# Kernel optimization log

Hardware: AMD Instinct MI355X
Metric: run time of the kernel (lower is better)

## Reference

```python
import jax, jax.numpy as jnp
import numpy as np

N = 100_000            # nodes
E = 1_600_000          # edges per metapath
IN = 256               # input features
HEADS, DIM = 8, 16     # heads * dim = hidden_channels
HIDDEN = HEADS * DIM   # 128
OUT = 4                # classes
NEG_SLOPE = 0.2


def setup_inputs() -> dict:
    key = jax.random.key(0)
    ks = jax.random.split(key, 16)
    s = 1.0 / np.sqrt(HIDDEN)
    return {
        "x": jax.random.normal(ks[0], (N, IN), jnp.float32),
        "edge_index0": jax.random.randint(ks[1], (2, E), 0, N, jnp.int64),
        "edge_index1": jax.random.randint(ks[2], (2, E), 0, N, jnp.int64),
        "proj_w": jax.random.normal(ks[3], (IN, HIDDEN), jnp.float32) / np.sqrt(IN),
        "proj_b": jnp.zeros((HIDDEN,), jnp.float32),
        "att_src0": jax.random.normal(ks[4], (HEADS, DIM), jnp.float32) * s,
        "att_dst0": jax.random.normal(ks[5], (HEADS, DIM), jnp.float32) * s,
        "att_src1": jax.random.normal(ks[6], (HEADS, DIM), jnp.float32) * s,
        "att_dst1": jax.random.normal(ks[7], (HEADS, DIM), jnp.float32) * s,
        "k_lin_w": jax.random.normal(ks[8], (HIDDEN, HIDDEN), jnp.float32) * s,
        "k_lin_b": jnp.zeros((HIDDEN,), jnp.float32),
        "q": jax.random.normal(ks[9], (HIDDEN,), jnp.float32) * s,
        "lin_w": jax.random.normal(ks[10], (HIDDEN, OUT), jnp.float32) * s,
        "lin_b": jnp.zeros((OUT,), jnp.float32),
    }


def _metapath_conv(xp, a_src, a_dst, src, dst):
    # xp: [N,H,D]; a_src, a_dst: [H,D]; src/dst: [E]
    alpha_src = (xp * a_src).sum(-1)                     # [N,H]
    alpha_dst = (xp * a_dst).sum(-1)                     # [N,H]
    e = jax.nn.leaky_relu(alpha_src[src] + alpha_dst[dst], NEG_SLOPE)  # [E,H]
    emax = jax.ops.segment_max(e, dst, num_segments=N)  # [N,H] (stable softmax)
    e = jnp.exp(e - emax[dst])
    denom = jax.ops.segment_sum(e, dst, num_segments=N)
    alpha = e / (denom[dst] + 1e-16)                     # edge softmax per dst
    msg = xp[src] * alpha[..., None]                     # [E,H,D]
    out = jax.ops.segment_sum(msg, dst, num_segments=N)  # [N,H,D]
    return jax.nn.relu(out.reshape(N, HIDDEN))


def reference(x, edge_index0, edge_index1, proj_w, proj_b,
              att_src0, att_dst0, att_src1, att_dst1,
              k_lin_w, k_lin_b, q, lin_w, lin_b):
    # shared node-type projection
    xp = (x @ proj_w + proj_b).reshape(N, HEADS, DIM)
    # per-metapath GAT-style convolutions (dropout=0.6 is eval no-op)
    outs = jnp.stack([
        _metapath_conv(xp, att_src0, att_dst0, edge_index0[0], edge_index0[1]),
        _metapath_conv(xp, att_src1, att_dst1, edge_index1[0], edge_index1[1]),
    ])                                                    # [M,N,HIDDEN]
    # semantic attention over metapaths
    k = jnp.tanh(outs @ k_lin_w + k_lin_b).mean(axis=1)  # [M,HIDDEN]
    attn = jax.nn.softmax((k * q).sum(-1))               # [M]
    fused = (attn[:, None, None] * outs).sum(0)          # [N,HIDDEN]
    return fused @ lin_w + lin_b                          # [N,OUT]
```

## Files before the change

kernel.cpp:

```cpp
#include <hip/hip_runtime.h>
#include <hip/hip_bf16.h>

#define NN 100000
#define EE 1600000
#define HID 128
#define NEG 0.2f
#define CAP 64
#define BSH 9
#define NB 196
#define CAPB 9216
#define EBLK 16384

typedef __attribute__((ext_vector_type(8))) short short8;
typedef __attribute__((ext_vector_type(4))) float f32x4;

__global__ __launch_bounds__(256) void k_proj(const float* __restrict__ x,
    const float* __restrict__ w, const float* __restrict__ bias,
    __hip_bfloat162* __restrict__ xph) {
  __shared__ float xs[64][32];
  __shared__ float ws[32][128];
  const int tid = threadIdx.x;
  const int row0 = blockIdx.x * 64;
  const int cb = (tid & 31) * 4;
  const int rb = (tid >> 5) * 8;
  float acc[8][4] = {};
  for (int k0 = 0; k0 < 256; k0 += 32) {
    {
      int f = tid * 8;
      int r = f >> 5, c = f & 31;
      int rg = row0 + r;
      float4 v0 = make_float4(0.f, 0.f, 0.f, 0.f), v1 = v0;
      if (rg < NN) {
        const float4* src = (const float4*)&x[(size_t)rg * 256 + k0 + c];
        v0 = src[0];
        v1 = src[1];
      }
      *(float4*)&xs[r][c] = v0;
      *(float4*)&xs[r][c + 4] = v1;
    }
    {
      int f = tid * 16;
      int r = f >> 7, c = f & 127;
      const float4* src = (const float4*)&w[(size_t)(k0 + r) * 128 + c];
      float4 a0 = src[0], a1 = src[1], a2 = src[2], a3 = src[3];
      *(float4*)&ws[r][c] = a0;
      *(float4*)&ws[r][c + 4] = a1;
      *(float4*)&ws[r][c + 8] = a2;
      *(float4*)&ws[r][c + 12] = a3;
    }
    __syncthreads();
#pragma unroll
    for (int kk = 0; kk < 32; kk++) {
      float4 wv = *(const float4*)&ws[kk][cb];
#pragma unroll
      for (int r = 0; r < 8; r++) {
        float a = xs[rb + r][kk];
        acc[r][0] = fmaf(a, wv.x, acc[r][0]);
        acc[r][1] = fmaf(a, wv.y, acc[r][1]);
        acc[r][2] = fmaf(a, wv.z, acc[r][2]);
        acc[r][3] = fmaf(a, wv.w, acc[r][3]);
      }
    }
    __syncthreads();
  }
  float4 bv = *(const float4*)&bias[cb];
#pragma unroll
  for (int r = 0; r < 8; r++) {
    int rg = row0 + rb + r;
    if (rg < NN) {
      float4 o;
      o.x = acc[r][0] + bv.x;
      o.y = acc[r][1] + bv.y;
      o.z = acc[r][2] + bv.z;
      o.w = acc[r][3] + bv.w;
      __hip_bfloat162 b01 = __float22bfloat162_rn(make_float2(o.x, o.y));
      __hip_bfloat162 b23 = __float22bfloat162_rn(make_float2(o.z, o.w));
      *(uint2*)&xph[(size_t)rg * 64 + (cb >> 1)] =
          make_uint2(*(unsigned*)&b01, *(unsigned*)&b23);
    }
  }
}

__global__ __launch_bounds__(256) void k_alpha(const __hip_bfloat162* __restrict__ xph,
    const float* __restrict__ a0s, const float* __restrict__ a0d,
    const float* __restrict__ a1s, const float* __restrict__ a1d,
    float* __restrict__ as0, float* __restrict__ ad0,
    float* __restrict__ as1, float* __restrict__ ad1) {
  const int lane = threadIdx.x & 63;
  const int node = blockIdx.x * 4 + (threadIdx.x >> 6);
  if (node >= NN) return;
  float2 v = __bfloat1622float2(xph[(size_t)node * 64 + lane]);
  int i0 = 2 * lane;
  float p0 = v.x * a0s[i0] + v.y * a0s[i0 + 1];
  float p1 = v.x * a0d[i0] + v.y * a0d[i0 + 1];
  float p2 = v.x * a1s[i0] + v.y * a1s[i0 + 1];
  float p3 = v.x * a1d[i0] + v.y * a1d[i0 + 1];
#pragma unroll
  for (int off = 1; off < 8; off <<= 1) {
    p0 += __shfl_xor(p0, off, 64);
    p1 += __shfl_xor(p1, off, 64);
    p2 += __shfl_xor(p2, off, 64);
    p3 += __shfl_xor(p3, off, 64);
  }
  if ((lane & 7) == 0) {
    int h = lane >> 3;
    as0[node * 8 + h] = p0;
    ad0[node * 8 + h] = p1;
    as1[node * 8 + h] = p2;
    ad1[node * 8 + h] = p3;
  }
}

__global__ __launch_bounds__(256) void k_bin(const int* __restrict__ ei0,
    const int* __restrict__ ei1, int* __restrict__ gcur, int* __restrict__ binned) {
  const int p = blockIdx.y;
  const int* __restrict__ ei = p ? ei1 : ei0;
  const int* __restrict__ src = ei;
  const int* __restrict__ dst = ei + EE;
  int* __restrict__ gc = gcur + p * 256;
  int* __restrict__ bn = binned + (size_t)p * NB * CAPB;
  __shared__ int cntL[NB], baseL[NB], posL[NB];
  const int t = threadIdx.x;
  const int e0 = blockIdx.x * EBLK;
  const int e1 = min(e0 + EBLK, EE);
  for (int i = t; i < NB; i += 256) { cntL[i] = 0; posL[i] = 0; }
  __syncthreads();
  for (int e = e0 + t; e < e1; e += 256)
    atomicAdd(&cntL[dst[e] >> BSH], 1);
  __syncthreads();
  for (int i = t; i < NB; i += 256)
    baseL[i] = atomicAdd(&gc[i], cntL[i]);
  __syncthreads();
  for (int e = e0 + t; e < e1; e += 256) {
    int d = dst[e];
    int b = d >> BSH;
    int off = baseL[b] + atomicAdd(&posL[b], 1);
    if (off < CAPB) bn[b * CAPB + off] = (src[e] << BSH) | (d & 511);
  }
}

__global__ __launch_bounds__(256) void k_build(const int* __restrict__ gcur,
    const int* __restrict__ binned, int* __restrict__ cnt, int* __restrict__ csr) {
  const int p = blockIdx.y, b = blockIdx.x, t = threadIdx.x;
  const int* __restrict__ bn = binned + (size_t)p * NB * CAPB + (size_t)b * CAPB;
  const int n = min(gcur[p * 256 + b], CAPB);
  int* __restrict__ cs = csr + (size_t)p * NN * CAP;
  __shared__ int lc[512];
  lc[t] = 0;
  lc[t + 256] = 0;
  __syncthreads();
  const int node0 = b << BSH;
  for (int i = t; i < n; i += 256) {
    int v = bn[i];
    int ln = v & 511;
    int off = atomicAdd(&lc[ln], 1);
    if (off < CAP) cs[(size_t)(node0 + ln) * CAP + off] = v >> BSH;
  }
  __syncthreads();
  int n0 = node0 + t, n1 = node0 + t + 256;
  if (n0 < NN) cnt[p * NN + n0] = lc[t];
  if (n1 < NN) cnt[p * NN + n1] = lc[t + 256];
}

#define LRELU(t) ((t) > 0.f ? (t) : NEG * (t))

#define EDGE_BODY(sv)                                      \
  {                                                        \
    unsigned s = (unsigned)(sv);                           \
    float t = asrc[s * 8u + h];                            \
    __hip_bfloat162 v = xph[s * 64u + lane];               \
    float al = __expf(LRELU(t + ad));                      \
    denom += al;                                           \
    float2 f = __bfloat1622float2(v);                      \
    a0 = fmaf(al, f.x, a0);                                \
    a1 = fmaf(al, f.y, a1);                                \
  }

__global__ __launch_bounds__(256) void k_aggr(const __hip_bfloat162* __restrict__ xph,
    const float* __restrict__ as0, const float* __restrict__ ad0,
    const float* __restrict__ as1, const float* __restrict__ ad1,
    const int* __restrict__ cnt, const int* __restrict__ csr,
    __hip_bfloat162* __restrict__ h0, __hip_bfloat162* __restrict__ h1) {
  const int p = blockIdx.y;
  const unsigned lane = threadIdx.x & 63;
  const int node = blockIdx.x * 4 + (threadIdx.x >> 6);
  if (node >= NN) return;
  const float* __restrict__ asrc = p ? as1 : as0;
  const float* __restrict__ adst = p ? ad1 : ad0;
  const int* __restrict__ cs = csr + ((size_t)p * NN + node) * CAP;
  __hip_bfloat162* __restrict__ hout = p ? h1 : h0;
  const unsigned h = lane >> 3;
  const float ad = adst[(unsigned)node * 8u + h];
  const int deg = min(cnt[p * NN + node], CAP);

  float denom = 1e-16f, a0 = 0.f, a1 = 0.f;
  int e = 0;
  for (; e + 8 <= deg; e += 8) {
    int4 q0 = *(const int4*)&cs[e];
    int4 q1 = *(const int4*)&cs[e + 4];
    EDGE_BODY(q0.x) EDGE_BODY(q0.y) EDGE_BODY(q0.z) EDGE_BODY(q0.w)
    EDGE_BODY(q1.x) EDGE_BODY(q1.y) EDGE_BODY(q1.z) EDGE_BODY(q1.w)
  }
  for (; e + 4 <= deg; e += 4) {
    int4 q0 = *(const int4*)&cs[e];
    EDGE_BODY(q0.x) EDGE_BODY(q0.y) EDGE_BODY(q0.z) EDGE_BODY(q0.w)
  }
  for (; e < deg; e++) EDGE_BODY(cs[e])
  float inv = 1.f / denom;
  hout[(size_t)node * 64 + lane] =
      __float22bfloat162_rn(make_float2(fmaxf(a0 * inv, 0.f), fmaxf(a1 * inv, 0.f)));
}

#define KWS 136
#define NTILES ((NN + 63) / 64)
#define SEMGX 256

__global__ __launch_bounds__(256) void k_sem(const __hip_bfloat16* __restrict__ h0,
    const __hip_bfloat16* __restrict__ h1, const float* __restrict__ kw,
    const float* __restrict__ kb, float* __restrict__ ksum) {
  __shared__ short kwT[128 * KWS];
  __shared__ float red[4][128];
  const int tid = threadIdx.x;
  const int m = blockIdx.y;
  const short* __restrict__ hc = (const short*)(m ? h1 : h0);
  for (int l = tid; l < 128 * 128; l += 256) {
    int i = l >> 7, j = l & 127;
    __hip_bfloat16 bv = __float2bfloat16(kw[l]);
    kwT[j * KWS + i] = *(short*)&bv;
  }
  const int lane = tid & 63;
  const int wave = tid >> 6;
  const int rowgrp = lane >> 4;
  const int lcol = lane & 15;
  float partial[8] = {};
  float kbv[8];
#pragma unroll
  for (int ct = 0; ct < 8; ct++) kbv[ct] = kb[ct * 16 + lcol];
  __syncthreads();
  for (int tile = blockIdx.x; tile < NTILES; tile += SEMGX) {
    int n0 = tile * 64 + wave * 16;
    int row = n0 + lcol;
    if (row >= NN) row = 0;
    const short* hr = hc + (size_t)row * 128 + rowgrp * 8;
    short8 afrag[4];
#pragma unroll
    for (int kc = 0; kc < 4; kc++) afrag[kc] = *(const short8*)(hr + kc * 32);
#pragma unroll
    for (int ct = 0; ct < 8; ct++) {
      f32x4 acc = {0.f, 0.f, 0.f, 0.f};
#pragma unroll
      for (int kc = 0; kc < 4; kc++) {
        short8 bfrag = *(const short8*)&kwT[(ct * 16 + lcol) * KWS + kc * 32 + rowgrp * 8];
        acc = __builtin_amdgcn_mfma_f32_16x16x32_bf16(afrag[kc], bfrag, acc, 0, 0, 0);
      }
#pragma unroll
      for (int r = 0; r < 4; r++) {
        int node = n0 + rowgrp * 4 + r;
        if (node < NN) partial[ct] += tanhf(acc[r] + kbv[ct]);
      }
    }
  }
#pragma unroll
  for (int ct = 0; ct < 8; ct++) {
    partial[ct] += __shfl_xor(partial[ct], 16, 64);
    partial[ct] += __shfl_xor(partial[ct], 32, 64);
  }
  if (lane < 16) {
#pragma unroll
    for (int ct = 0; ct < 8; ct++) red[wave][ct * 16 + lane] = partial[ct];
  }
  __syncthreads();
  if (tid < 128) {
    float s = red[0][tid] + red[1][tid] + red[2][tid] + red[3][tid];
    atomicAdd(&ksum[m * 128 + tid], s);
  }
}

__global__ void k_attn(const float* __restrict__ ksum, const float* __restrict__ q,
                       float* __restrict__ attn) {
  __shared__ float red0[128], red1[128];
  int t = threadIdx.x;
  float qv = q[t];
  red0[t] = ksum[t] * qv;
  red1[t] = ksum[128 + t] * qv;
  __syncthreads();
  for (int off = 64; off > 0; off >>= 1) {
    if (t < off) {
      red0[t] += red0[t + off];
      red1[t] += red1[t + off];
    }
    __syncthreads();
  }
  if (t == 0) {
    float l0 = red0[0] / (float)NN, l1 = red1[0] / (float)NN;
    float mx = fmaxf(l0, l1);
    float e0 = __expf(l0 - mx), e1 = __expf(l1 - mx);
    float s = e0 + e1;
    attn[0] = e0 / s;
    attn[1] = e1 / s;
  }
}

__global__ __launch_bounds__(256) void k_final(const __hip_bfloat162* __restrict__ h0,
    const __hip_bfloat162* __restrict__ h1, const float* __restrict__ lw,
    const float* __restrict__ lb, const float* __restrict__ attn,
    float* __restrict__ out) {
  const int lane = threadIdx.x & 63;
  const int node = blockIdx.x * 4 + (threadIdx.x >> 6);
  if (node >= NN) return;
  float a0 = attn[0], a1 = attn[1];
  float2 v0 = __bfloat1622float2(h0[(size_t)node * 64 + lane]);
  float2 v1 = __bfloat1622float2(h1[(size_t)node * 64 + lane]);
  float f0 = a0 * v0.x + a1 * v1.x;
  float f1 = a0 * v0.y + a1 * v1.y;
  int i0 = 2 * lane;
  float p[4];
#pragma unroll
  for (int c = 0; c < 4; c++)
    p[c] = f0 * lw[i0 * 4 + c] + f1 * lw[(i0 + 1) * 4 + c];
#pragma unroll
  for (int off = 32; off > 0; off >>= 1) {
#pragma unroll
    for (int c = 0; c < 4; c++) p[c] += __shfl_down(p[c], off, 64);
  }
  if (lane == 0) {
#pragma unroll
    for (int c = 0; c < 4; c++) out[(size_t)node * 4 + c] = p[c] + lb[c];
  }
}

extern "C" void kernel_launch(void* const* d_in, const int* in_sizes, int n_in,
                              void* d_out, int out_size, void* d_ws, size_t ws_size,
                              hipStream_t stream) {
  const float* x      = (const float*)d_in[0];
  const int*   ei0    = (const int*)d_in[1];
  const int*   ei1    = (const int*)d_in[2];
  const float* proj_w = (const float*)d_in[3];
  const float* proj_b = (const float*)d_in[4];
  const float* a0s    = (const float*)d_in[5];
  const float* a0d    = (const float*)d_in[6];
  const float* a1s    = (const float*)d_in[7];
  const float* a1d    = (const float*)d_in[8];
  const float* klw    = (const float*)d_in[9];
  const float* klb    = (const float*)d_in[10];
  const float* q      = (const float*)d_in[11];
  const float* lw     = (const float*)d_in[12];
  const float* lb     = (const float*)d_in[13];
  float* out = (float*)d_out;

  char* ws = (char*)d_ws;
  size_t off = 0;
  auto alloc = [&](size_t bytes) -> void* {
    size_t o = (off + 255) & ~(size_t)255;
    off = o + bytes;
    return (void*)(ws + o);
  };
  __hip_bfloat162* xph = (__hip_bfloat162*)alloc((size_t)NN * 128 * 2);
  __hip_bfloat162* h0  = (__hip_bfloat162*)alloc((size_t)NN * 128 * 2);
  __hip_bfloat162* h1  = (__hip_bfloat162*)alloc((size_t)NN * 128 * 2);
  float* as0  = (float*)alloc((size_t)NN * 8 * 4);
  float* ad0  = (float*)alloc((size_t)NN * 8 * 4);
  float* as1  = (float*)alloc((size_t)NN * 8 * 4);
  float* ad1  = (float*)alloc((size_t)NN * 8 * 4);
  int* cnt    = (int*)alloc((size_t)2 * NN * 4);
  float* ksum = (float*)alloc(256 * 4);
  int* gcur   = (int*)alloc(2 * 256 * 4);
  float* attn = (float*)alloc(256);
  int* csr    = (int*)alloc((size_t)2 * NN * CAP * 4);
  int* binned = (int*)alloc((size_t)2 * NB * CAPB * 4);

  hipMemsetAsync(cnt, 0, (size_t)2 * NN * 4 + 256 * 4 + 2 * 256 * 4, stream);

  k_proj<<<dim3((NN + 63) / 64), 256, 0, stream>>>(x, proj_w, proj_b, xph);
  k_alpha<<<dim3((NN + 3) / 4), 256, 0, stream>>>(xph, a0s, a0d, a1s, a1d,
                                                  as0, ad0, as1, ad1);
  k_bin<<<dim3((EE + EBLK - 1) / EBLK, 2), 256, 0, stream>>>(ei0, ei1, gcur, binned);
  k_build<<<dim3(NB, 2), 256, 0, stream>>>(gcur, binned, cnt, csr);
  k_aggr<<<dim3((NN + 3) / 4, 2), 256, 0, stream>>>(xph, as0, ad0, as1, ad1,
                                                    cnt, csr, h0, h1);
  k_sem<<<dim3(SEMGX, 2), 256, 0, stream>>>((const __hip_bfloat16*)h0,
                                            (const __hip_bfloat16*)h1, klw, klb, ksum);
  k_attn<<<dim3(1), 128, 0, stream>>>(ksum, q, attn);
  k_final<<<dim3((NN + 3) / 4), 256, 0, stream>>>(h0, h1, lw, lb, attn, out);
}
```

Measured before the change: 588.0 us.

## Use bf16 MFMA projection, cooperative edge aggregation, wider build blocks, smaller bin chunks

The input projection moves from an fp32 SIMT tiled GEMM to bf16 MFMA 16x16x32 in a persistent grid, with the weight transposed into LDS once per block. The aggregation kernel now loads 8 edges' source indices and attention logits in parallel across lane groups and broadcasts them with shuffles, so each lane no longer does serial index and logit loads per edge. k_build uses 512 threads and k_bin uses 4096-edge chunks for more blocks. The projection now rounds inputs to bf16, which lowers accuracy, and the shuffle-heavy aggregation adds cross-lane work.

```diff
diff --git a/kernel.cpp b/kernel.cpp
--- a/kernel.cpp
+++ b/kernel.cpp
@@ -9,74 +9,63 @@
 #define BSH 9
 #define NB 196
 #define CAPB 9216
-#define EBLK 16384
+#define EBLK 4096
 
 typedef __attribute__((ext_vector_type(8))) short short8;
 typedef __attribute__((ext_vector_type(4))) float f32x4;
 
+#define PWS 264
+#define PNT ((NN + 15) / 16)
+
 __global__ __launch_bounds__(256) void k_proj(const float* __restrict__ x,
     const float* __restrict__ w, const float* __restrict__ bias,
-    __hip_bfloat162* __restrict__ xph) {
-  __shared__ float xs[64][32];
-  __shared__ float ws[32][128];
+    __hip_bfloat16* __restrict__ xph) {
+  __shared__ short wT[128 * PWS];
   const int tid = threadIdx.x;
-  const int row0 = blockIdx.x * 64;
-  const int cb = (tid & 31) * 4;
-  const int rb = (tid >> 5) * 8;
-  float acc[8][4] = {};
-  for (int k0 = 0; k0 < 256; k0 += 32) {
-    {
-      int f = tid * 8;
-      int r = f >> 5, c = f & 31;
-      int rg = row0 + r;
-      float4 v0 = make_float4(0.f, 0.f, 0.f, 0.f), v1 = v0;
-      if (rg < NN) {
-        const float4* src = (const float4*)&x[(size_t)rg * 256 + k0 + c];
-        v0 = src[0];
-        v1 = src[1];
+  for (int l = tid; l < 256 * 128; l += 256) {
+    int k = l >> 7, n = l & 127;
+    __hip_bfloat16 bv = __float2bfloat16(w[l]);
+    wT[n * PWS + k] = *(short*)&bv;
+  }
+  const int lane = tid & 63, wave = tid >> 6;
+  const int rowgrp = lane >> 4, lcol = lane & 15;
+  float bv[8];
+#pragma unroll
+  for (int ct = 0; ct < 8; ct++) bv[ct] = bias[ct * 16 + lcol];
+  __syncthreads();
+  for (int tile = blockIdx.x * 4 + wave; tile < PNT; tile += gridDim.x * 4) {
+    const int r0 = tile * 16;
+    int row = r0 + lcol;
+    if (row >= NN) row = NN - 1;
+    const float* xr = x + (size_t)row * 256 + rowgrp * 8;
+    short8 af[8];
+#pragma unroll
+    for (int kc = 0; kc < 8; kc++) {
+      float4 u0 = *(const float4*)(xr + kc * 32);
+      float4 u1 = *(const float4*)(xr + kc * 32 + 4);
+      union { short8 v; __hip_bfloat162 h[4]; } u;
+      u.h[0] = __float22bfloat162_rn(make_float2(u0.x, u0.y));
+      u.h[1] = __float22bfloat162_rn(make_float2(u0.z, u0.w));
+      u.h[2] = __float22bfloat162_rn(make_float2(u1.x, u1.y));
+      u.h[3] = __float22bfloat162_rn(make_float2(u1.z, u1.w));
+      af[kc] = u.v;
+    }
+#pragma unroll
+    for (int ct = 0; ct < 8; ct++) {
+      f32x4 acc = {0.f, 0.f, 0.f, 0.f};
+#pragma unroll
+      for (int kc = 0; kc < 8; kc++) {
+        short8 bf = *(const short8*)&wT[(ct * 16 + lcol) * PWS + kc * 32 + rowgrp * 8];
+        acc = __builtin_amdgcn_mfma_f32_16x16x32_bf16(af[kc], bf, acc, 0, 0, 0);
       }
-      *(float4*)&xs[r][c] = v0;
-      *(float4*)&xs[r][c + 4] = v1;
-    }
-    {
-      int f = tid * 16;
-      int r = f >> 7, c = f & 127;
-      const float4* src = (const float4*)&w[(size_t)(k0 + r) * 128 + c];
-      float4 a0 = src[0], a1 = src[1], a2 = src[2], a3 = src[3];
-      *(float4*)&ws[r][c] = a0;
-      *(float4*)&ws[r][c + 4] = a1;
-      *(float4*)&ws[r][c + 8] = a2;
-      *(float4*)&ws[r][c + 12] = a3;
-    }
-    __syncthreads();
-#pragma unroll
-    for (int kk = 0; kk < 32; kk++) {
-      float4 wv = *(const float4*)&ws[kk][cb];
-#pragma unroll
-      for (int r = 0; r < 8; r++) {
-        float a = xs[rb + r][kk];
-        acc[r][0] = fmaf(a, wv.x, acc[r][0]);
-        acc[r][1] = fmaf(a, wv.y, acc[r][1]);
-        acc[r][2] = fmaf(a, wv.z, acc[r][2]);
-        acc[r][3] = fmaf(a, wv.w, acc[r][3]);
+#pragma unroll
+      for (int r = 0; r < 4; r++) {
+        int orow = r0 + rowgrp * 4 + r;
+        if (orow < NN) {
+          __hip_bfloat16 ob = __float2bfloat16(acc[r] + bv[ct]);
+          ((short*)xph)[(size_t)orow * 128 + ct * 16 + lcol] = *(short*)&ob;
+        }
       }
-    }
-    __syncthreads();
-  }
-  float4 bv = *(const float4*)&bias[cb];
-#pragma unroll
-  for (int r = 0; r < 8; r++) {
-    int rg = row0 + rb + r;
-    if (rg < NN) {
-      float4 o;
-      o.x = acc[r][0] + bv.x;
-      o.y = acc[r][1] + bv.y;
-      o.z = acc[r][2] + bv.z;
-      o.w = acc[r][3] + bv.w;
-      __hip_bfloat162 b01 = __float22bfloat162_rn(make_float2(o.x, o.y));
-      __hip_bfloat162 b23 = __float22bfloat162_rn(make_float2(o.z, o.w));
-      *(uint2*)&xph[(size_t)rg * 64 + (cb >> 1)] =
-          make_uint2(*(unsigned*)&b01, *(unsigned*)&b23);
     }
   }
 }
@@ -139,7 +128,7 @@
   }
 }
 
-__global__ __launch_bounds__(256) void k_build(const int* __restrict__ gcur,
+__global__ __launch_bounds__(512) void k_build(const int* __restrict__ gcur,
     const int* __restrict__ binned, int* __restrict__ cnt, int* __restrict__ csr) {
   const int p = blockIdx.y, b = blockIdx.x, t = threadIdx.x;
   const int* __restrict__ bn = binned + (size_t)p * NB * CAPB + (size_t)b * CAPB;
@@ -147,34 +136,18 @@
   int* __restrict__ cs = csr + (size_t)p * NN * CAP;
   __shared__ int lc[512];
   lc[t] = 0;
-  lc[t + 256] = 0;
   __syncthreads();
   const int node0 = b << BSH;
-  for (int i = t; i < n; i += 256) {
+  for (int i = t; i < n; i += 512) {
     int v = bn[i];
     int ln = v & 511;
     int off = atomicAdd(&lc[ln], 1);
     if (off < CAP) cs[(size_t)(node0 + ln) * CAP + off] = v >> BSH;
   }
   __syncthreads();
-  int n0 = node0 + t, n1 = node0 + t + 256;
+  int n0 = node0 + t;
   if (n0 < NN) cnt[p * NN + n0] = lc[t];
-  if (n1 < NN) cnt[p * NN + n1] = lc[t + 256];
-}
-
-#define LRELU(t) ((t) > 0.f ? (t) : NEG * (t))
-
-#define EDGE_BODY(sv)                                      \
-  {                                                        \
-    unsigned s = (unsigned)(sv);                           \
-    float t = asrc[s * 8u + h];                            \
-    __hip_bfloat162 v = xph[s * 64u + lane];               \
-    float al = __expf(LRELU(t + ad));                      \
-    denom += al;                                           \
-    float2 f = __bfloat1622float2(v);                      \
-    a0 = fmaf(al, f.x, a0);                                \
-    a1 = fmaf(al, f.y, a1);                                \
-  }
+}
 
 __global__ __launch_bounds__(256) void k_aggr(const __hip_bfloat162* __restrict__ xph,
     const float* __restrict__ as0, const float* __restrict__ ad0,
@@ -182,31 +155,45 @@
     const int* __restrict__ cnt, const int* __restrict__ csr,
     __hip_bfloat162* __restrict__ h0, __hip_bfloat162* __restrict__ h1) {
   const int p = blockIdx.y;
-  const unsigned lane = threadIdx.x & 63;
+  const int lane = threadIdx.x & 63;
   const int node = blockIdx.x * 4 + (threadIdx.x >> 6);
   if (node >= NN) return;
   const float* __restrict__ asrc = p ? as1 : as0;
   const float* __restrict__ adst = p ? ad1 : ad0;
   const int* __restrict__ cs = csr + ((size_t)p * NN + node) * CAP;
   __hip_bfloat162* __restrict__ hout = p ? h1 : h0;
-  const unsigned h = lane >> 3;
-  const float ad = adst[(unsigned)node * 8u + h];
+  const int g = lane >> 3;
+  const int h8 = lane & 7;
+  const int hf = lane >> 3;
+  const float ad8 = adst[(unsigned)node * 8u + h8];
   const int deg = min(cnt[p * NN + node], CAP);
 
-  float denom = 1e-16f, a0 = 0.f, a1 = 0.f;
-  int e = 0;
-  for (; e + 8 <= deg; e += 8) {
-    int4 q0 = *(const int4*)&cs[e];
-    int4 q1 = *(const int4*)&cs[e + 4];
-    EDGE_BODY(q0.x) EDGE_BODY(q0.y) EDGE_BODY(q0.z) EDGE_BODY(q0.w)
-    EDGE_BODY(q1.x) EDGE_BODY(q1.y) EDGE_BODY(q1.z) EDGE_BODY(q1.w)
-  }
-  for (; e + 4 <= deg; e += 4) {
-    int4 q0 = *(const int4*)&cs[e];
-    EDGE_BODY(q0.x) EDGE_BODY(q0.y) EDGE_BODY(q0.z) EDGE_BODY(q0.w)
-  }
-  for (; e < deg; e++) EDGE_BODY(cs[e])
-  float inv = 1.f / denom;
+  float dsum = 0.f, a0 = 0.f, a1 = 0.f;
+  for (int e0 = 0; e0 < deg; e0 += 8) {
+    int idx = e0 + g;
+    bool valid = idx < deg;
+    int s8 = cs[valid ? idx : 0];
+    float t = asrc[(unsigned)s8 * 8u + h8];
+    float xv = t + ad8;
+    float al = __expf(fmaxf(xv, NEG * xv));
+    al = valid ? al : 0.f;
+    dsum += al;
+    const int nval = min(deg - e0, 8);
+#pragma unroll
+    for (int gp = 0; gp < 8; gp++) {
+      if (gp >= nval) break;
+      int sb = __shfl(s8, gp * 8, 64);
+      float ab = __shfl(al, gp * 8 + hf, 64);
+      float2 f = __bfloat1622float2(xph[(unsigned)sb * 64u + lane]);
+      a0 = fmaf(ab, f.x, a0);
+      a1 = fmaf(ab, f.y, a1);
+    }
+  }
+  dsum += __shfl_xor(dsum, 8, 64);
+  dsum += __shfl_xor(dsum, 16, 64);
+  dsum += __shfl_xor(dsum, 32, 64);
+  float denom = __shfl(dsum, hf, 64);
+  float inv = 1.f / (denom + 1e-16f);
   hout[(size_t)node * 64 + lane] =
       __float22bfloat162_rn(make_float2(fmaxf(a0 * inv, 0.f), fmaxf(a1 * inv, 0.f)));
 }
@@ -371,11 +358,11 @@
 
   hipMemsetAsync(cnt, 0, (size_t)2 * NN * 4 + 256 * 4 + 2 * 256 * 4, stream);
 
-  k_proj<<<dim3((NN + 63) / 64), 256, 0, stream>>>(x, proj_w, proj_b, xph);
+  k_proj<<<dim3(256), 256, 0, stream>>>(x, proj_w, proj_b, (__hip_bfloat16*)xph);
   k_alpha<<<dim3((NN + 3) / 4), 256, 0, stream>>>(xph, a0s, a0d, a1s, a1d,
                                                   as0, ad0, as1, ad1);
   k_bin<<<dim3((EE + EBLK - 1) / EBLK, 2), 256, 0, stream>>>(ei0, ei1, gcur, binned);
-  k_build<<<dim3(NB, 2), 256, 0, stream>>>(gcur, binned, cnt, csr);
+  k_build<<<dim3(NB, 2), 512, 0, stream>>>(gcur, binned, cnt, csr);
   k_aggr<<<dim3((NN + 3) / 4, 2), 256, 0, stream>>>(xph, as0, ad0, as1, ad1,
                                                     cnt, csr, h0, h1);
   k_sem<<<dim3(SEMGX, 2), 256, 0, stream>>>((const __hip_bfloat16*)h0,
```

Result: slower. 618.1 us (+5.1%).
